# Kernel tuning notes

Hardware: AMD Instinct MI355X
Metric: run time of the kernel (lower is better)

The kernel has to match this reference:

```python
import jax, jax.numpy as jnp
import numpy as np

N = 500_000   # nodes
D = 128       # feature dim (init arg d)
B = 1024      # number of graphs / segments
EPS = 1e-6


def setup_inputs() -> dict:
    key = jax.random.key(0)
    k_x, k_b, k_ps, k_qs, k_w, k_bias = jax.random.split(key, 6)
    x = jax.random.normal(k_x, (N, D), dtype=jnp.float32)
    batch = jnp.sort(jax.random.randint(k_b, (N,), 0, B)).astype(jnp.int64)
    ps_raw = jax.random.normal(k_ps, (2,), dtype=jnp.float32)
    qs_raw = jax.random.normal(k_qs, (2,), dtype=jnp.float32)
    W = jax.random.normal(k_w, (D, D), dtype=jnp.float32) / np.sqrt(D)
    b = jax.random.normal(k_bias, (D,), dtype=jnp.float32) * 0.01
    return {"x": x, "batch": batch, "ps_raw": ps_raw, "qs_raw": qs_raw, "W": W, "b": b}


def reference(x, batch, ps_raw, qs_raw, W, b):
    # ps = -Threshold(thr=-50, val=50)(-softplus(ps_raw))
    sp = jax.nn.softplus(ps_raw)
    ps = -jnp.where(-sp > -50.0, -sp, 50.0)
    qs = jnp.tanh(qs_raw)

    # per-graph node counts: global_add_pool(ones)
    nums = jax.ops.segment_sum(jnp.ones(x.shape[0], dtype=x.dtype), batch,
                               num_segments=B)[:, None]            # (B, 1)

    xa = jnp.abs(x) + EPS                                           # (N, D)
    d1 = xa.shape[1] // 2                                           # split feature dim

    # positive branch: exp(p0 * log(x)) == x**p0, summed per graph
    x_pos = jnp.exp(ps[0] * jnp.log(xa[:, :d1]))                    # (N, d1)
    s_pos = jax.ops.segment_sum(x_pos, batch, num_segments=B)       # (B, d1)
    gnp_pos = jnp.exp(jnp.log(s_pos) / ps[0]) / nums ** qs[0]

    # negative branch: plain power / root p-norm form
    s_neg = jax.ops.segment_sum(xa[:, d1:] ** ps[1], batch, num_segments=B)  # (B, D-d1)
    gnp_neg = s_neg ** (1.0 / ps[1]) / nums ** qs[0]

    gnp = jnp.concatenate([gnp_pos, gnp_neg], axis=1)               # (B, D)
    return gnp @ W.T + b
```

## Files before the change

kernel.cpp:

```cpp
#include <hip/hip_runtime.h>
#include <math.h>

#define NSEG   1024
#define DFEAT  128
#define EPS_F  1e-6f

__device__ __forceinline__ float softplus_thr(float v) {
    float sp = log1pf(__expf(v));
    return (sp >= 50.0f) ? -50.0f : sp;
}

__global__ __launch_bounds__(512, 8)
void fused_pool_kernel(const float* __restrict__ x,
                       const int*   __restrict__ batch,
                       const float* __restrict__ ps_raw,
                       const float* __restrict__ qs_raw,
                       const float* __restrict__ W,
                       const float* __restrict__ bias,
                       float* __restrict__ out,
                       int n_nodes)
{
    const int b    = blockIdx.x;
    const int tid  = threadIdx.x;
    const int w    = tid >> 6;
    const int lane = tid & 63;
    const int half = lane >> 5;
    const int f4   = lane & 31;

    int lo0 = 0, hi0 = n_nodes;
    int lo1 = 0, hi1 = n_nodes;
    while (lo0 < hi0) { int m = (lo0 + hi0) >> 1; if (batch[m] < b)     lo0 = m + 1; else hi0 = m; }
    while (lo1 < hi1) { int m = (lo1 + hi1) >> 1; if (batch[m] < b + 1) lo1 = m + 1; else hi1 = m; }
    const int start = lo0, end = lo1;

    const float p = softplus_thr(ps_raw[(f4 < 16) ? 0 : 1]);

    const float4* __restrict__ x4 = (const float4*)x;
    float a0 = 0.f, a1 = 0.f, a2 = 0.f, a3 = 0.f;
#pragma unroll 2
    for (int r = start + 2 * w + half; r < end; r += 16) {
        const float4 v = x4[(size_t)r * 32 + f4];
        a0 += __expf(p * __logf(fabsf(v.x) + EPS_F));
        a1 += __expf(p * __logf(fabsf(v.y) + EPS_F));
        a2 += __expf(p * __logf(fabsf(v.z) + EPS_F));
        a3 += __expf(p * __logf(fabsf(v.w) + EPS_F));
    }

    __shared__ float part[16][DFEAT + 4];
    __shared__ float g[DFEAT];
    float4* dst = (float4*)&part[2 * w + half][4 * f4];
    *dst = make_float4(a0, a1, a2, a3);
    __syncthreads();

    if (tid < DFEAT) {
        float ssum = 0.f;
#pragma unroll
        for (int k = 0; k < 16; ++k) ssum += part[k][tid];
        const float pf = softplus_thr(ps_raw[(tid < 64) ? 0 : 1]);
        const float q0 = tanhf(qs_raw[0]);
        const float n  = (float)(end - start);
        g[tid] = __expf(__logf(ssum) / pf - q0 * __logf(n));
    }
    __syncthreads();

    if (tid >= DFEAT) return;

    const float4* __restrict__ W4 = (const float4*)(W + (size_t)tid * DFEAT);
    const float4* g4 = (const float4*)g;
    float acc = bias[tid];
#pragma unroll
    for (int jj = 0; jj < DFEAT / 4; ++jj) {
        const float4 wv = W4[jj];
        const float4 gv = g4[jj];
        acc += gv.x * wv.x + gv.y * wv.y + gv.z * wv.z + gv.w * wv.w;
    }
    out[(size_t)b * DFEAT + tid] = acc;
}

extern "C" void kernel_launch(void* const* d_in, const int* in_sizes, int n_in,
                              void* d_out, int out_size, void* d_ws, size_t ws_size,
                              hipStream_t stream)
{
    const float* x      = (const float*)d_in[0];
    const int*   batch  = (const int*)  d_in[1];
    const float* ps_raw = (const float*)d_in[2];
    const float* qs_raw = (const float*)d_in[3];
    const float* W      = (const float*)d_in[4];
    const float* bias   = (const float*)d_in[5];
    float*       out    = (float*)d_out;

    const int n_nodes = in_sizes[0] / DFEAT;

    fused_pool_kernel<<<NSEG, 512, 0, stream>>>(x, batch, ps_raw, qs_raw,
                                                W, bias, out, n_nodes);
}
```

Baseline: 370.3 us.

## Split segment pooling into balanced row-chunk pass plus finalize kernel

Replaces the one-block-per-segment pooling with a two-kernel scheme. The first kernel processes equal row chunks across 2048 blocks, keeps boundary-segment partials in per-chunk buffers, and atomically adds interior segment sums into a workspace. A second kernel combines the chunk partials, applies the power/normalization and does the GEMV with W. This is meant to remove load imbalance from uneven segment sizes and improve occupancy, at the cost of an extra launch, global atomics and workspace traffic.

After: 374.9 us. Within noise of the previous version (+1.2%).

```diff
diff --git a/kernel.cpp b/kernel.cpp
--- a/kernel.cpp
+++ b/kernel.cpp
@@ -4,77 +4,145 @@
 #define NSEG   1024
 #define DFEAT  128
 #define EPS_F  1e-6f
+#define NBLK_A 2048
+#define THR_A  256
 
 __device__ __forceinline__ float softplus_thr(float v) {
     float sp = log1pf(__expf(v));
     return (sp >= 50.0f) ? -50.0f : sp;
 }
 
-__global__ __launch_bounds__(512, 8)
-void fused_pool_kernel(const float* __restrict__ x,
-                       const int*   __restrict__ batch,
-                       const float* __restrict__ ps_raw,
-                       const float* __restrict__ qs_raw,
-                       const float* __restrict__ W,
-                       const float* __restrict__ bias,
-                       float* __restrict__ out,
-                       int n_nodes)
+__global__ __launch_bounds__(THR_A, 8)
+void segsum_chunk_kernel(const float* __restrict__ x,
+                         const int*   __restrict__ batch,
+                         const float* __restrict__ ps_raw,
+                         float* __restrict__ pcF,
+                         float* __restrict__ pcL,
+                         int*   __restrict__ idFL,
+                         float* __restrict__ sMid,
+                         int n_nodes, int chunk)
 {
-    const int b    = blockIdx.x;
-    const int tid  = threadIdx.x;
-    const int w    = tid >> 6;
-    const int lane = tid & 63;
-    const int half = lane >> 5;
-    const int f4   = lane & 31;
+    const int k   = blockIdx.x;
+    const int tid = threadIdx.x;
+    const int hw  = tid >> 5;
+    const int f4  = tid & 31;
+    const int r0  = k * chunk;
 
-    int lo0 = 0, hi0 = n_nodes;
-    int lo1 = 0, hi1 = n_nodes;
+    if (r0 >= n_nodes) {
+        if (tid == 0) { idFL[2 * k] = -1; idFL[2 * k + 1] = -1; }
+        return;
+    }
+    const int r1  = min(r0 + chunk, n_nodes);
+    const int idF = batch[r0];
+    const int idL = batch[r1 - 1];
+    if (tid == 0) { idFL[2 * k] = idF; idFL[2 * k + 1] = idL; }
+
+    for (int sg = idF + 1 + hw; sg < idL; sg += 8) {
+        float4* p = (float4*)&sMid[(size_t)sg * DFEAT];
+        p[f4] = make_float4(0.f, 0.f, 0.f, 0.f);
+    }
+    __syncthreads();
+
+    const float p = softplus_thr(ps_raw[(f4 < 16) ? 0 : 1]);
+    const float4* __restrict__ x4 = (const float4*)x;
+
+    float4 aF  = make_float4(0.f, 0.f, 0.f, 0.f);
+    float4 aL  = make_float4(0.f, 0.f, 0.f, 0.f);
+    float4 acc = make_float4(0.f, 0.f, 0.f, 0.f);
+
+    auto flush = [&](int seg) {
+        if (seg == idF) {
+            aF.x += acc.x; aF.y += acc.y; aF.z += acc.z; aF.w += acc.w;
+        } else if (seg == idL) {
+            aL.x += acc.x; aL.y += acc.y; aL.z += acc.z; aL.w += acc.w;
+        } else {
+            float* base = &sMid[(size_t)seg * DFEAT + 4 * f4];
+            atomicAdd(base + 0, acc.x); atomicAdd(base + 1, acc.y);
+            atomicAdd(base + 2, acc.z); atomicAdd(base + 3, acc.w);
+        }
+        acc = make_float4(0.f, 0.f, 0.f, 0.f);
+    };
+
+    int rfirst = r0 + hw;
+    int cur = (rfirst < r1) ? batch[rfirst] : idF;
+
+#pragma unroll 2
+    for (int r = rfirst; r < r1; r += 8) {
+        const int sg = batch[r];
+        if (sg != cur) { flush(cur); cur = sg; }
+        const float4 v = x4[(size_t)r * 32 + f4];
+        acc.x += __expf(p * __logf(fabsf(v.x) + EPS_F));
+        acc.y += __expf(p * __logf(fabsf(v.y) + EPS_F));
+        acc.z += __expf(p * __logf(fabsf(v.z) + EPS_F));
+        acc.w += __expf(p * __logf(fabsf(v.w) + EPS_F));
+    }
+    flush(cur);
+
+    __shared__ float pFs[8][DFEAT];
+    __shared__ float pLs[8][DFEAT];
+    *(float4*)&pFs[hw][4 * f4] = aF;
+    *(float4*)&pLs[hw][4 * f4] = aL;
+    __syncthreads();
+
+    if (tid < DFEAT) {
+        float sF = 0.f, sL = 0.f;
+#pragma unroll
+        for (int j = 0; j < 8; ++j) { sF += pFs[j][tid]; sL += pLs[j][tid]; }
+        pcF[(size_t)k * DFEAT + tid] = sF;
+        pcL[(size_t)k * DFEAT + tid] = sL;
+    }
+}
+
+__global__ __launch_bounds__(128)
+void finalize_gemm_kernel(const int*   __restrict__ batch,
+                          const float* __restrict__ pcF,
+                          const float* __restrict__ pcL,
+                          const int*   __restrict__ idFL,
+                          const float* __restrict__ sMid,
+                          const float* __restrict__ ps_raw,
+                          const float* __restrict__ qs_raw,
+                          const float* __restrict__ W,
+                          const float* __restrict__ bias,
+                          float* __restrict__ out,
+                          int n_nodes, int chunk, int nblk)
+{
+    const int b = blockIdx.x;
+    const int i = threadIdx.x;
+
+    int lo0 = 0, hi0 = n_nodes, lo1 = 0, hi1 = n_nodes;
     while (lo0 < hi0) { int m = (lo0 + hi0) >> 1; if (batch[m] < b)     lo0 = m + 1; else hi0 = m; }
     while (lo1 < hi1) { int m = (lo1 + hi1) >> 1; if (batch[m] < b + 1) lo1 = m + 1; else hi1 = m; }
     const int start = lo0, end = lo1;
 
-    const float p = softplus_thr(ps_raw[(f4 < 16) ? 0 : 1]);
-
-    const float4* __restrict__ x4 = (const float4*)x;
-    float a0 = 0.f, a1 = 0.f, a2 = 0.f, a3 = 0.f;
-#pragma unroll 2
-    for (int r = start + 2 * w + half; r < end; r += 16) {
-        const float4 v = x4[(size_t)r * 32 + f4];
-        a0 += __expf(p * __logf(fabsf(v.x) + EPS_F));
-        a1 += __expf(p * __logf(fabsf(v.y) + EPS_F));
-        a2 += __expf(p * __logf(fabsf(v.z) + EPS_F));
-        a3 += __expf(p * __logf(fabsf(v.w) + EPS_F));
+    float ssum = 0.f;
+    if (end > start) {
+        const int ks = start / chunk;
+        const int ke = (end - 1) / chunk;
+        for (int k = ks; k <= ke && k < nblk; ++k) {
+            const int f = idFL[2 * k], l = idFL[2 * k + 1];
+            if (f == b)                 ssum += pcF[(size_t)k * DFEAT + i];
+            else if (f < b && b < l)    ssum += sMid[(size_t)b * DFEAT + i];
+            if (l == b && l != f)       ssum += pcL[(size_t)k * DFEAT + i];
+        }
     }
 
-    __shared__ float part[16][DFEAT + 4];
     __shared__ float g[DFEAT];
-    float4* dst = (float4*)&part[2 * w + half][4 * f4];
-    *dst = make_float4(a0, a1, a2, a3);
+    const float pf = softplus_thr(ps_raw[(i < 64) ? 0 : 1]);
+    const float q0 = tanhf(qs_raw[0]);
+    const float n  = (float)(end - start);
+    g[i] = __expf(__logf(ssum) / pf - q0 * __logf(n));
     __syncthreads();
 
-    if (tid < DFEAT) {
-        float ssum = 0.f;
-#pragma unroll
-        for (int k = 0; k < 16; ++k) ssum += part[k][tid];
-        const float pf = softplus_thr(ps_raw[(tid < 64) ? 0 : 1]);
-        const float q0 = tanhf(qs_raw[0]);
-        const float n  = (float)(end - start);
-        g[tid] = __expf(__logf(ssum) / pf - q0 * __logf(n));
-    }
-    __syncthreads();
-
-    if (tid >= DFEAT) return;
-
-    const float4* __restrict__ W4 = (const float4*)(W + (size_t)tid * DFEAT);
+    const float4* __restrict__ W4 = (const float4*)(W + (size_t)i * DFEAT);
     const float4* g4 = (const float4*)g;
-    float acc = bias[tid];
+    float acc = bias[i];
 #pragma unroll
     for (int jj = 0; jj < DFEAT / 4; ++jj) {
         const float4 wv = W4[jj];
         const float4 gv = g4[jj];
         acc += gv.x * wv.x + gv.y * wv.y + gv.z * wv.z + gv.w * wv.w;
     }
-    out[(size_t)b * DFEAT + tid] = acc;
+    out[(size_t)b * DFEAT + i] = acc;
 }
 
 extern "C" void kernel_launch(void* const* d_in, const int* in_sizes, int n_in,
@@ -90,7 +158,16 @@
     float*       out    = (float*)d_out;
 
     const int n_nodes = in_sizes[0] / DFEAT;
+    const int chunk   = (n_nodes + NBLK_A - 1) / NBLK_A;
 
-    fused_pool_kernel<<<NSEG, 512, 0, stream>>>(x, batch, ps_raw, qs_raw,
-                                                W, bias, out, n_nodes);
+    float* pcF  = (float*)d_ws;
+    float* pcL  = pcF  + (size_t)NBLK_A * DFEAT;
+    float* sMid = pcL  + (size_t)NBLK_A * DFEAT;
+    int*   idFL = (int*)(sMid + (size_t)NSEG * DFEAT);
+
+    segsum_chunk_kernel<<<NBLK_A, THR_A, 0, stream>>>(
+        x, batch, ps_raw, pcF, pcL, idFL, sMid, n_nodes, chunk);
+    finalize_gemm_kernel<<<NSEG, 128, 0, stream>>>(
+        batch, pcF, pcL, idFL, sMid, ps_raw, qs_raw, W, bias, out,
+        n_nodes, chunk, NBLK_A);
 }
```
